# Kernel tuning notes

Measured on AMD Instinct MI355X. Metric: run time of the kernel, lower is better.

## Reference

```python
import jax, jax.numpy as jnp
import numpy as np

B_SZ, L, H, P, V, OUT_LEN = 32, 4096, 512, 384, 32, 16
DT_MIN, DT_MAX = 0.001, 0.1


def setup_inputs() -> dict:
    key = jax.random.key(0)
    ks = jax.random.split(key, 12)
    tokens = jax.random.randint(ks[0], (B_SZ, L), 0, V, dtype=jnp.int32)
    embed = jax.random.normal(ks[1], (V, H), dtype=jnp.float32) * 0.02
    # S5 diagonal state: Lambda = Lambda_re + i*Lambda_im (stable: Re < 0)
    Lambda_re = -0.5 * jax.random.uniform(ks[2], (P,), dtype=jnp.float32) - 1e-3
    Lambda_im = jnp.pi * jnp.arange(P, dtype=jnp.float32)
    B_re = jax.random.normal(ks[3], (P, H), dtype=jnp.float32) / np.sqrt(H)
    B_im = jax.random.normal(ks[4], (P, H), dtype=jnp.float32) / np.sqrt(H)
    C_re = jax.random.normal(ks[5], (H, P), dtype=jnp.float32) / np.sqrt(P)
    C_im = jax.random.normal(ks[6], (H, P), dtype=jnp.float32) / np.sqrt(P)
    D = jax.random.normal(ks[7], (H,), dtype=jnp.float32)
    log_step = jax.random.uniform(
        ks[8], (P,), dtype=jnp.float32,
        minval=np.log(DT_MIN), maxval=np.log(DT_MAX))
    W1 = jax.random.normal(ks[9], (H, H), dtype=jnp.float32) / np.sqrt(H)
    b1 = jnp.zeros((H,), dtype=jnp.float32)
    W2 = jax.random.normal(ks[10], (H, V), dtype=jnp.float32) / np.sqrt(H)
    b2 = jnp.zeros((V,), dtype=jnp.float32)
    return dict(tokens=tokens, embed=embed, Lambda_re=Lambda_re,
                Lambda_im=Lambda_im, B_re=B_re, B_im=B_im, C_re=C_re,
                C_im=C_im, D=D, log_step=log_step, W1=W1, b1=b1, W2=W2, b2=b2)


def _s5_scan(Lbar, Bu_bar):
    # Lbar: (P,) complex; Bu_bar: (B,L,P) complex
    A = jnp.broadcast_to(Lbar, Bu_bar.shape)

    def comb(e1, e2):
        A1, b1 = e1
        A2, b2 = e2
        return A2 * A1, A2 * b1 + b2

    _, xs = jax.lax.associative_scan(comb, (A, Bu_bar), axis=1)
    return xs  # (B,L,P) hidden states


def reference(tokens, embed, Lambda_re, Lambda_im, B_re, B_im,
              C_re, C_im, D, log_step, W1, b1, W2, b2):
    u = embed[tokens]                              # (B,L,H) real
    Lam = Lambda_re + 1j * Lambda_im               # (P,)
    step = jnp.exp(log_step)                       # (P,)
    Lbar = jnp.exp(Lam * step)                     # ZOH: exp(Lambda*dt)
    Bc = B_re + 1j * B_im                          # (P,H)
    Cc = C_re + 1j * C_im                          # (H,P)
    Bu = jnp.einsum('blh,ph->blp', u, Bc)          # (B,L,P) complex
    Bu_bar = ((Lbar - 1.0) / Lam) * Bu             # ZOH input discretization
    xs = _s5_scan(Lbar, Bu_bar)                    # (B,L,P)
    # conj_sym=True -> 2 * Re(C x) + D u
    y = 2.0 * jnp.einsum('blp,hp->blh', xs, Cc).real + u * D
    y = y[:, -OUT_LEN:, :]                         # (B,16,H)
    h = jax.nn.relu(y @ W1 + b1)
    return h @ W2 + b2                             # (B,16,V)
```

## Files before the change

### kernel.cpp

```cpp
#include <hip/hip_runtime.h>

#define B_SZ 32
#define L 4096
#define H 512
#define P 384
#define V 32
#define OUT_LEN 16
#define NC 48
#define CHUNK 85
#define T0 4080

#define OFF_DBL   0
#define OFF_LBARF 4608
#define OFF_WPOW  5376
#define OFF_M     79104
#define OFF_CT    103680
#define OFF_PART  496896
#define OFF_YT    1676544
#define OFF_HP    1938688

__global__ __launch_bounds__(256) void k_prep(
    const int* __restrict__ tokens, const float* __restrict__ embed,
    const float* __restrict__ Lre, const float* __restrict__ Lim,
    const float* __restrict__ Bre, const float* __restrict__ Bim,
    const float* __restrict__ Cre, const float* __restrict__ Cim,
    const float* __restrict__ log_step, float* __restrict__ ws)
{
    __shared__ float sre[32][33], sim[32][33];
    int bx = blockIdx.x, tid = threadIdx.x;
    if (bx < 2) {
        int p = bx * 256 + tid;
        if (p < P) {
            double dstep = exp((double)log_step[p]);
            double are = (double)Lre[p] * dstep, aim = (double)Lim[p] * dstep;
            double mag = exp(are);
            double lbr = mag * cos(aim), lbi = mag * sin(aim);
            double wmag = exp((double)CHUNK * are);
            double wang = (double)CHUNK * aim;
            double wr = wmag * cos(wang), wi = wmag * sin(wang);
            double lre = (double)Lre[p], lim = (double)Lim[p];
            double nr = lbr - 1.0, ni = lbi;
            double den = lre * lre + lim * lim;
            double cr = (nr * lre + ni * lim) / den, ci = (ni * lre - nr * lim) / den;
            double* d = (double*)ws + p * 6;
            d[0] = lbr; d[1] = lbi; d[2] = wr; d[3] = wi; d[4] = cr; d[5] = ci;
            ws[OFF_LBARF + 2 * p]     = (float)lbr;
            ws[OFF_LBARF + 2 * p + 1] = (float)lbi;
            double* wpow = (double*)(ws + OFF_WPOW);
            double awr = 1.0, awi = 0.0;
            for (int c = NC - 1; c >= 0; --c) {
                wpow[(c * P + p) * 2]     = awr;
                wpow[(c * P + p) * 2 + 1] = awi;
                double t = awr * wr - awi * wi;
                awi = awr * wi + awi * wr;
                awr = t;
            }
        }
    } else if (bx < 194) {
        int bxx = bx - 2;
        int tp = bxx >> 4, th = bxx & 15;
        int col = tid & 31, r0 = tid >> 5;
        #pragma unroll
        for (int it = 0; it < 4; ++it) {
            int row = r0 + 8 * it;
            int h = th * 32 + row, p = tp * 32 + col;
            sre[col][row] = Cre[h * P + p];
            sim[col][row] = Cim[h * P + p];
        }
        __syncthreads();
        #pragma unroll
        for (int it = 0; it < 4; ++it) {
            int pl = r0 + 8 * it;
            int p = tp * 32 + pl, h = th * 32 + col;
            ws[OFF_CT + (2 * p) * H + h]     = sre[pl][col];
            ws[OFF_CT + (2 * p + 1) * H + h] = sim[pl][col];
        }
    }
    {
        int w = bx * 4 + (tid >> 6);
        if (w < 1536) {
            int v0 = (w & 3) * 8, p = w >> 2;
            int lane = tid & 63;
            const float4* brp = (const float4*)(Bre + p * H);
            const float4* bip = (const float4*)(Bim + p * H);
            float4 br0 = brp[lane], br1 = brp[lane + 64];
            float4 bi0 = bip[lane], bi1 = bip[lane + 64];
            #pragma unroll
            for (int vv = 0; vv < 8; ++vv) {
                const float4* evp = (const float4*)(embed + (v0 + vv) * H);
                float4 e0 = evp[lane], e1 = evp[lane + 64];
                float dr = br0.x * e0.x;
                dr = fmaf(br0.y, e0.y, dr); dr = fmaf(br0.z, e0.z, dr);
                dr = fmaf(br0.w, e0.w, dr); dr = fmaf(br1.x, e1.x, dr);
                dr = fmaf(br1.y, e1.y, dr); dr = fmaf(br1.z, e1.z, dr);
                dr = fmaf(br1.w, e1.w, dr);
                float di = bi0.x * e0.x;
                di = fmaf(bi0.y, e0.y, di); di = fmaf(bi0.z, e0.z, di);
                di = fmaf(bi0.w, e0.w, di); di = fmaf(bi1.x, e1.x, di);
                di = fmaf(bi1.y, e1.y, di); di = fmaf(bi1.z, e1.z, di);
                di = fmaf(bi1.w, e1.w, di);
                #pragma unroll
                for (int off = 32; off; off >>= 1) {
                    dr += __shfl_down(dr, off);
                    di += __shfl_down(di, off);
                }
                if (lane == 0) {
                    ws[OFF_M + ((v0 + vv) * P + p) * 2]     = dr;
                    ws[OFF_M + ((v0 + vv) * P + p) * 2 + 1] = di;
                }
            }
        }
    }
}

__global__ __launch_bounds__(256) void k_scan(
    const int* __restrict__ tokens, const float* __restrict__ ws,
    float* __restrict__ part)
{
    __shared__ float2 sM[V * 192];
    int rem = blockIdx.x, b = blockIdx.y, tid = threadIdx.x;
    int ph = rem & 1;
    int c0 = (rem >> 1) * 4;
    const float2* Mg = (const float2*)(ws + OFF_M);
    for (int f = tid; f < V * 192; f += 256) {
        int v = f / 192, i = f - v * 192;
        sM[f] = Mg[v * P + ph * 192 + i];
    }
    __syncthreads();
    if (tid < 192) {
        int p = ph * 192 + tid;
        float Lr = ws[OFF_LBARF + 2 * p], Li = ws[OFF_LBARF + 2 * p + 1];
        const int* tk0 = tokens + b * L + (c0 + 0) * CHUNK;
        const int* tk1 = tokens + b * L + (c0 + 1) * CHUNK;
        const int* tk2 = tokens + b * L + (c0 + 2) * CHUNK;
        const int* tk3 = tokens + b * L + (c0 + 3) * CHUNK;
        float ar0 = 0, ai0 = 0, ar1 = 0, ai1 = 0;
        float ar2 = 0, ai2 = 0, ar3 = 0, ai3 = 0;
        for (int i = 0; i < CHUNK; ++i) {
            int t0 = tk0[i], t1 = tk1[i], t2 = tk2[i], t3 = tk3[i];
            float2 m0 = sM[t0 * 192 + tid];
            float2 m1 = sM[t1 * 192 + tid];
            float2 m2 = sM[t2 * 192 + tid];
            float2 m3 = sM[t3 * 192 + tid];
            float n;
            n = fmaf(Lr, ar0, fmaf(-Li, ai0, m0.x));
            ai0 = fmaf(Lr, ai0, fmaf(Li, ar0, m0.y)); ar0 = n;
            n = fmaf(Lr, ar1, fmaf(-Li, ai1, m1.x));
            ai1 = fmaf(Lr, ai1, fmaf(Li, ar1, m1.y)); ar1 = n;
            n = fmaf(Lr, ar2, fmaf(-Li, ai2, m2.x));
            ai2 = fmaf(Lr, ai2, fmaf(Li, ar2, m2.y)); ar2 = n;
            n = fmaf(Lr, ar3, fmaf(-Li, ai3, m3.x));
            ai3 = fmaf(Lr, ai3, fmaf(Li, ar3, m3.y)); ar3 = n;
        }
        const double* wpow = (const double*)(ws + OFF_WPOW);
        float* pt = part;
        #pragma unroll
        for (int k = 0; k < 4; ++k) {
            double wr = wpow[((c0 + k) * P + p) * 2];
            double wi = wpow[((c0 + k) * P + p) * 2 + 1];
            double ar = (k == 0) ? ar0 : (k == 1) ? ar1 : (k == 2) ? ar2 : ar3;
            double ai = (k == 0) ? ai0 : (k == 1) ? ai1 : (k == 2) ? ai2 : ai3;
            double sr = wr * ar - wi * ai;
            double si = wr * ai + wi * ar;
            pt[((b * NC + c0 + k) * P + p) * 2]     = (float)sr;
            pt[((b * NC + c0 + k) * P + p) * 2 + 1] = (float)si;
        }
    }
}

__global__ __launch_bounds__(256) void k_y(
    const int* __restrict__ tokens, const float* __restrict__ embed,
    const float* __restrict__ D, float* __restrict__ ws)
{
    __shared__ float sxs[P * 16];
    __shared__ float sred[4 * 64 * 9];
    int bx = blockIdx.x, tid = threadIdx.x;
    int b = bx >> 4, x = bx & 15;
    int lh = x & 1, hq = x >> 1;
    #pragma unroll
    for (int pass = 0; pass < 2; ++pass) {
        int p = tid + pass * 256;
        if (p < P) {
            const double* d = (const double*)ws + p * 6;
            double lbr = d[0], lbi = d[1], cr = d[4], ci = d[5];
            const float* pp = ws + OFF_PART + (b * NC * P + p) * 2;
            double s0r = 0, s0i = 0, s1r = 0, s1i = 0;
            double s2r = 0, s2i = 0, s3r = 0, s3i = 0;
            #pragma unroll
            for (int c = 0; c < NC; c += 4) {
                s0r += (double)pp[(c + 0) * P * 2];
                s0i += (double)pp[(c + 0) * P * 2 + 1];
                s1r += (double)pp[(c + 1) * P * 2];
                s1i += (double)pp[(c + 1) * P * 2 + 1];
                s2r += (double)pp[(c + 2) * P * 2];
                s2i += (double)pp[(c + 2) * P * 2 + 1];
                s3r += (double)pp[(c + 3) * P * 2];
                s3i += (double)pp[(c + 3) * P * 2 + 1];
            }
            double zr = (s0r + s1r) + (s2r + s3r);
            double zi = (s0i + s1i) + (s2i + s3i);
            const float* M0 = ws + OFF_M;
            const int* tk = tokens + b * L + T0;
            #pragma unroll
            for (int j = 0; j < OUT_LEN; ++j) {
                int t = tk[j];
                double mr = (double)M0[(t * P + p) * 2];
                double mi = (double)M0[(t * P + p) * 2 + 1];
                double tr = lbr * zr - lbi * zi + mr;
                double ti = lbr * zi + lbi * zr + mi;
                zr = tr; zi = ti;
                if ((j >> 3) == lh) {
                    int jl = j & 7;
                    sxs[p * 16 + 2 * jl]     = (float)(cr * zr - ci * zi);
                    sxs[p * 16 + 2 * jl + 1] = (float)(cr * zi + ci * zr);
                }
            }
        }
    }
    __syncthreads();
    int hl = tid & 63, pg = tid >> 6;
    int h = hq * 64 + hl;
    const float* ct = ws + OFF_CT;
    float acc[8];
    #pragma unroll
    for (int i = 0; i < 8; ++i) acc[i] = 0.f;
    int p0 = pg * 96;
    #pragma unroll 2
    for (int q = 0; q < 96; ++q) {
        int p = p0 + q;
        float cre = ct[(2 * p) * H + h];
        float cim = ct[(2 * p + 1) * H + h];
        const float4* xv = (const float4*)(sxs + p * 16);
        float4 x0 = xv[0], x1 = xv[1], x2 = xv[2], x3 = xv[3];
        acc[0] = fmaf(cre, x0.x, fmaf(-cim, x0.y, acc[0]));
        acc[1] = fmaf(cre, x0.z, fmaf(-cim, x0.w, acc[1]));
        acc[2] = fmaf(cre, x1.x, fmaf(-cim, x1.y, acc[2]));
        acc[3] = fmaf(cre, x1.z, fmaf(-cim, x1.w, acc[3]));
        acc[4] = fmaf(cre, x2.x, fmaf(-cim, x2.y, acc[4]));
        acc[5] = fmaf(cre, x2.z, fmaf(-cim, x2.w, acc[5]));
        acc[6] = fmaf(cre, x3.x, fmaf(-cim, x3.y, acc[6]));
        acc[7] = fmaf(cre, x3.z, fmaf(-cim, x3.w, acc[7]));
    }
    #pragma unroll
    for (int i = 0; i < 8; ++i)
        sred[(pg * 64 + hl) * 9 + i] = acc[i];
    __syncthreads();
    #pragma unroll
    for (int oo = 0; oo < 2; ++oo) {
        int o = tid + 256 * oo;
        int ohl = o & 63, oi = o >> 6;
        float s = sred[ohl * 9 + oi] + sred[(64 + ohl) * 9 + oi]
                + sred[(128 + ohl) * 9 + oi] + sred[(192 + ohl) * 9 + oi];
        int l = lh * 8 + oi;
        int t = tokens[b * L + T0 + l];
        int hh = hq * 64 + ohl;
        ws[OFF_YT + (b * OUT_LEN + l) * H + hh] =
            2.f * s + embed[t * H + hh] * D[hh];
    }
}

__global__ __launch_bounds__(256) void k_fc1(
    const float* __restrict__ W1, const float* __restrict__ ws,
    float* __restrict__ hp)
{
    __shared__ float ys[128 * 8];
    int bx = blockIdx.x, tid = threadIdx.x;
    int rg = bx >> 3, jh = (bx >> 2) & 1, kc = bx & 3;
    int j = jh * 256 + tid;
    int r0 = rg * 8, k0 = kc * 128;
    const float* yt = ws + OFF_YT;
    int kk = tid & 127, rr = tid >> 7;
    #pragma unroll
    for (int it = 0; it < 4; ++it)
        ys[kk * 8 + rr + 2 * it] = yt[(r0 + rr + 2 * it) * H + k0 + kk];
    __syncthreads();
    const float* wp = W1 + k0 * H + j;
    float wreg[8];
    #pragma unroll
    for (int u = 0; u < 8; ++u) wreg[u] = wp[u * H];
    float acc[8] = {0, 0, 0, 0, 0, 0, 0, 0};
    for (int kb = 0; kb < 128; kb += 8) {
        float cur[8];
        #pragma unroll
        for (int u = 0; u < 8; ++u) cur[u] = wreg[u];
        if (kb + 8 < 128) {
            #pragma unroll
            for (int u = 0; u < 8; ++u) wreg[u] = wp[(kb + 8 + u) * H];
        }
        #pragma unroll
        for (int u = 0; u < 8; ++u) {
            const float4* y0 = (const float4*)(ys + (kb + u) * 8);
            float4 p0 = y0[0], p1 = y0[1];
            float a = cur[u];
            acc[0] = fmaf(p0.x, a, acc[0]);
            acc[1] = fmaf(p0.y, a, acc[1]);
            acc[2] = fmaf(p0.z, a, acc[2]);
            acc[3] = fmaf(p0.w, a, acc[3]);
            acc[4] = fmaf(p1.x, a, acc[4]);
            acc[5] = fmaf(p1.y, a, acc[5]);
            acc[6] = fmaf(p1.z, a, acc[6]);
            acc[7] = fmaf(p1.w, a, acc[7]);
        }
    }
    #pragma unroll
    for (int i = 0; i < 8; ++i)
        hp[(kc * 512 + r0 + i) * H + j] = acc[i];
}

__global__ __launch_bounds__(256) void k_fc2(
    const float* __restrict__ b1, const float* __restrict__ W2,
    const float* __restrict__ b2, const float* __restrict__ hp,
    float* __restrict__ out)
{
    __shared__ float sh[512];
    __shared__ float red[8 * 32];
    int r = blockIdx.x, tid = threadIdx.x;
    #pragma unroll
    for (int half = 0; half < 2; ++half) {
        int j = half * 256 + tid;
        float s = b1[j] + hp[r * H + j] + hp[(512 + r) * H + j]
                        + hp[(1024 + r) * H + j] + hp[(1536 + r) * H + j];
        sh[j] = fmaxf(s, 0.f);
    }
    __syncthreads();
    int seg = tid >> 5, o = tid & 31;
    const float* w2 = W2 + seg * 64 * V + o;
    const float* hv = sh + seg * 64;
    float a0 = 0.f, a1 = 0.f, a2 = 0.f, a3 = 0.f;
    #pragma unroll
    for (int q = 0; q < 16; ++q) {
        a0 = fmaf(hv[q],      w2[q * V],        a0);
        a1 = fmaf(hv[16 + q], w2[(16 + q) * V], a1);
        a2 = fmaf(hv[32 + q], w2[(32 + q) * V], a2);
        a3 = fmaf(hv[48 + q], w2[(48 + q) * V], a3);
    }
    red[seg * 32 + o] = (a0 + a1) + (a2 + a3);
    __syncthreads();
    if (tid < 32) {
        float s = b2[tid];
        #pragma unroll
        for (int ss = 0; ss < 8; ++ss) s += red[ss * 32 + tid];
        out[r * V + tid] = s;
    }
}

extern "C" void kernel_launch(void* const* d_in, const int* in_sizes, int n_in,
                              void* d_out, int out_size, void* d_ws, size_t ws_size,
                              hipStream_t stream)
{
    const int*   tokens = (const int*)d_in[0];
    const float* embed  = (const float*)d_in[1];
    const float* Lre    = (const float*)d_in[2];
    const float* Lim    = (const float*)d_in[3];
    const float* Bre    = (const float*)d_in[4];
    const float* Bim    = (const float*)d_in[5];
    const float* Cre    = (const float*)d_in[6];
    const float* Cim    = (const float*)d_in[7];
    const float* D      = (const float*)d_in[8];
    const float* lstep  = (const float*)d_in[9];
    const float* W1     = (const float*)d_in[10];
    const float* b1     = (const float*)d_in[11];
    const float* W2     = (const float*)d_in[12];
    const float* b2     = (const float*)d_in[13];
    float* out = (float*)d_out;
    float* ws  = (float*)d_ws;

    k_prep<<<384, 256, 0, stream>>>(tokens, embed, Lre, Lim, Bre, Bim,
                                    Cre, Cim, lstep, ws);
    k_scan<<<dim3(24, 32), 256, 0, stream>>>(tokens, ws, ws + OFF_PART);
    k_y   <<<512, 256, 0, stream>>>(tokens, embed, D, ws);
    k_fc1 <<<512, 256, 0, stream>>>(W1, ws, ws + OFF_HP);
    k_fc2 <<<512, 256, 0, stream>>>(b1, W2, b2, ws + OFF_HP, out);
}
```

Baseline: 148.0 us.

## Interleave scan by stride-4 lanes, reduce superchunks via atomics, prefetch C in k_y

The scan now splits each sequence into 12 superchunks of 340 tokens. Each superchunk is processed as four interleaved sub-sequences, using Lbar^4 as the recurrence factor and reading tokens with int4 loads. The four partial states are recombined in double precision with powers of Lbar, weighted by the superchunk power, and summed with float atomicAdd into a per-batch accumulator. This replaces the per-chunk partial array and the 48-way reduction in k_y. The C-projection loop in k_y also gains software prefetching of C values. The risks are atomic contention, run-to-run nondeterminism in the sum, and the accuracy of float Lbar^4 over long runs.

```diff
diff --git a/kernel.cpp b/kernel.cpp
--- a/kernel.cpp
+++ b/kernel.cpp
@@ -6,21 +6,22 @@
 #define P 384
 #define V 32
 #define OUT_LEN 16
-#define NC 48
-#define CHUNK 85
+#define NSC 12
+#define SCLEN 340
+#define NSTEP 85
 #define T0 4080
 
 #define OFF_DBL   0
-#define OFF_LBARF 4608
+#define OFF_LBF4  4608
 #define OFF_WPOW  5376
-#define OFF_M     79104
-#define OFF_CT    103680
-#define OFF_PART  496896
-#define OFF_YT    1676544
-#define OFF_HP    1938688
+#define OFF_M     23808
+#define OFF_CT    48384
+#define OFF_XACC  441600
+#define OFF_YT    466176
+#define OFF_HP    728320
 
 __global__ __launch_bounds__(256) void k_prep(
-    const int* __restrict__ tokens, const float* __restrict__ embed,
+    const float* __restrict__ embed,
     const float* __restrict__ Lre, const float* __restrict__ Lim,
     const float* __restrict__ Bre, const float* __restrict__ Bim,
     const float* __restrict__ Cre, const float* __restrict__ Cim,
@@ -28,6 +29,7 @@
 {
     __shared__ float sre[32][33], sim[32][33];
     int bx = blockIdx.x, tid = threadIdx.x;
+    if (bx < 96) ws[OFF_XACC + bx * 256 + tid] = 0.f;
     if (bx < 2) {
         int p = bx * 256 + tid;
         if (p < P) {
@@ -35,20 +37,21 @@
             double are = (double)Lre[p] * dstep, aim = (double)Lim[p] * dstep;
             double mag = exp(are);
             double lbr = mag * cos(aim), lbi = mag * sin(aim);
-            double wmag = exp((double)CHUNK * are);
-            double wang = (double)CHUNK * aim;
-            double wr = wmag * cos(wang), wi = wmag * sin(wang);
             double lre = (double)Lre[p], lim = (double)Lim[p];
             double nr = lbr - 1.0, ni = lbi;
             double den = lre * lre + lim * lim;
             double cr = (nr * lre + ni * lim) / den, ci = (ni * lre - nr * lim) / den;
             double* d = (double*)ws + p * 6;
-            d[0] = lbr; d[1] = lbi; d[2] = wr; d[3] = wi; d[4] = cr; d[5] = ci;
-            ws[OFF_LBARF + 2 * p]     = (float)lbr;
-            ws[OFF_LBARF + 2 * p + 1] = (float)lbi;
+            d[0] = lbr; d[1] = lbi; d[2] = 0.0; d[3] = 0.0; d[4] = cr; d[5] = ci;
+            double m4 = exp(4.0 * are), a4 = 4.0 * aim;
+            ws[OFF_LBF4 + 2 * p]     = (float)(m4 * cos(a4));
+            ws[OFF_LBF4 + 2 * p + 1] = (float)(m4 * sin(a4));
+            double wmag = exp((double)SCLEN * are);
+            double wang = (double)SCLEN * aim;
+            double wr = wmag * cos(wang), wi = wmag * sin(wang);
             double* wpow = (double*)(ws + OFF_WPOW);
             double awr = 1.0, awi = 0.0;
-            for (int c = NC - 1; c >= 0; --c) {
+            for (int c = NSC - 1; c >= 0; --c) {
                 wpow[(c * P + p) * 2]     = awr;
                 wpow[(c * P + p) * 2 + 1] = awi;
                 double t = awr * wr - awi * wi;
@@ -114,13 +117,12 @@
 }
 
 __global__ __launch_bounds__(256) void k_scan(
-    const int* __restrict__ tokens, const float* __restrict__ ws,
-    float* __restrict__ part)
+    const int* __restrict__ tokens, float* __restrict__ ws)
 {
     __shared__ float2 sM[V * 192];
-    int rem = blockIdx.x, b = blockIdx.y, tid = threadIdx.x;
-    int ph = rem & 1;
-    int c0 = (rem >> 1) * 4;
+    int x = blockIdx.x, b = blockIdx.y, tid = threadIdx.x;
+    int ph = x & 1;
+    int sc = x >> 1;
     const float2* Mg = (const float2*)(ws + OFF_M);
     for (int f = tid; f < V * 192; f += 256) {
         int v = f / 192, i = f - v * 192;
@@ -129,19 +131,19 @@
     __syncthreads();
     if (tid < 192) {
         int p = ph * 192 + tid;
-        float Lr = ws[OFF_LBARF + 2 * p], Li = ws[OFF_LBARF + 2 * p + 1];
-        const int* tk0 = tokens + b * L + (c0 + 0) * CHUNK;
-        const int* tk1 = tokens + b * L + (c0 + 1) * CHUNK;
-        const int* tk2 = tokens + b * L + (c0 + 2) * CHUNK;
-        const int* tk3 = tokens + b * L + (c0 + 3) * CHUNK;
+        float Lr = ws[OFF_LBF4 + 2 * p], Li = ws[OFF_LBF4 + 2 * p + 1];
+        const int4* tkb = (const int4*)(tokens + b * L + sc * SCLEN);
         float ar0 = 0, ai0 = 0, ar1 = 0, ai1 = 0;
         float ar2 = 0, ai2 = 0, ar3 = 0, ai3 = 0;
-        for (int i = 0; i < CHUNK; ++i) {
-            int t0 = tk0[i], t1 = tk1[i], t2 = tk2[i], t3 = tk3[i];
-            float2 m0 = sM[t0 * 192 + tid];
-            float2 m1 = sM[t1 * 192 + tid];
-            float2 m2 = sM[t2 * 192 + tid];
-            float2 m3 = sM[t3 * 192 + tid];
+        int4 tq = tkb[0];
+        #pragma unroll 5
+        for (int i = 0; i < NSTEP; ++i) {
+            int4 cur = tq;
+            if (i + 1 < NSTEP) tq = tkb[i + 1];
+            float2 m0 = sM[cur.x * 192 + tid];
+            float2 m1 = sM[cur.y * 192 + tid];
+            float2 m2 = sM[cur.z * 192 + tid];
+            float2 m3 = sM[cur.w * 192 + tid];
             float n;
             n = fmaf(Lr, ar0, fmaf(-Li, ai0, m0.x));
             ai0 = fmaf(Lr, ai0, fmaf(Li, ar0, m0.y)); ar0 = n;
@@ -152,19 +154,20 @@
             n = fmaf(Lr, ar3, fmaf(-Li, ai3, m3.x));
             ai3 = fmaf(Lr, ai3, fmaf(Li, ar3, m3.y)); ar3 = n;
         }
+        const double* d = (const double*)ws + p * 6;
+        double l1r = d[0], l1i = d[1];
+        double l2r = l1r * l1r - l1i * l1i, l2i = 2.0 * l1r * l1i;
+        double l3r = l2r * l1r - l2i * l1i, l3i = l2r * l1i + l2i * l1r;
+        double zr = l3r * ar0 - l3i * ai0 + l2r * ar1 - l2i * ai1
+                  + l1r * ar2 - l1i * ai2 + (double)ar3;
+        double zi = l3r * ai0 + l3i * ar0 + l2r * ai1 + l2i * ar1
+                  + l1r * ai2 + l1i * ar2 + (double)ai3;
         const double* wpow = (const double*)(ws + OFF_WPOW);
-        float* pt = part;
-        #pragma unroll
-        for (int k = 0; k < 4; ++k) {
-            double wr = wpow[((c0 + k) * P + p) * 2];
-            double wi = wpow[((c0 + k) * P + p) * 2 + 1];
-            double ar = (k == 0) ? ar0 : (k == 1) ? ar1 : (k == 2) ? ar2 : ar3;
-            double ai = (k == 0) ? ai0 : (k == 1) ? ai1 : (k == 2) ? ai2 : ai3;
-            double sr = wr * ar - wi * ai;
-            double si = wr * ai + wi * ar;
-            pt[((b * NC + c0 + k) * P + p) * 2]     = (float)sr;
-            pt[((b * NC + c0 + k) * P + p) * 2 + 1] = (float)si;
-        }
+        double wr = wpow[(sc * P + p) * 2], wi = wpow[(sc * P + p) * 2 + 1];
+        float sr = (float)(wr * zr - wi * zi);
+        float si = (float)(wr * zi + wi * zr);
+        atomicAdd(ws + OFF_XACC + (b * P + p) * 2, sr);
+        atomicAdd(ws + OFF_XACC + (b * P + p) * 2 + 1, si);
     }
 }
 
@@ -183,22 +186,8 @@
         if (p < P) {
             const double* d = (const double*)ws + p * 6;
             double lbr = d[0], lbi = d[1], cr = d[4], ci = d[5];
-            const float* pp = ws + OFF_PART + (b * NC * P + p) * 2;
-            double s0r = 0, s0i = 0, s1r = 0, s1i = 0;
-            double s2r = 0, s2i = 0, s3r = 0, s3i = 0;
-            #pragma unroll
-            for (int c = 0; c < NC; c += 4) {
-                s0r += (double)pp[(c + 0) * P * 2];
-                s0i += (double)pp[(c + 0) * P * 2 + 1];
-                s1r += (double)pp[(c + 1) * P * 2];
-                s1i += (double)pp[(c + 1) * P * 2 + 1];
-                s2r += (double)pp[(c + 2) * P * 2];
-                s2i += (double)pp[(c + 2) * P * 2 + 1];
-                s3r += (double)pp[(c + 3) * P * 2];
-                s3i += (double)pp[(c + 3) * P * 2 + 1];
-            }
-            double zr = (s0r + s1r) + (s2r + s3r);
-            double zi = (s0i + s1i) + (s2i + s3i);
+            const float2 za = *(const float2*)(ws + OFF_XACC + (b * P + p) * 2);
+            double zr = (double)za.x, zi = (double)za.y;
             const float* M0 = ws + OFF_M;
             const int* tk = tokens + b * L + T0;
             #pragma unroll
@@ -225,21 +214,37 @@
     #pragma unroll
     for (int i = 0; i < 8; ++i) acc[i] = 0.f;
     int p0 = pg * 96;
-    #pragma unroll 2
-    for (int q = 0; q < 96; ++q) {
-        int p = p0 + q;
-        float cre = ct[(2 * p) * H + h];
-        float cim = ct[(2 * p + 1) * H + h];
-        const float4* xv = (const float4*)(sxs + p * 16);
-        float4 x0 = xv[0], x1 = xv[1], x2 = xv[2], x3 = xv[3];
-        acc[0] = fmaf(cre, x0.x, fmaf(-cim, x0.y, acc[0]));
-        acc[1] = fmaf(cre, x0.z, fmaf(-cim, x0.w, acc[1]));
-        acc[2] = fmaf(cre, x1.x, fmaf(-cim, x1.y, acc[2]));
-        acc[3] = fmaf(cre, x1.z, fmaf(-cim, x1.w, acc[3]));
-        acc[4] = fmaf(cre, x2.x, fmaf(-cim, x2.y, acc[4]));
-        acc[5] = fmaf(cre, x2.z, fmaf(-cim, x2.w, acc[5]));
-        acc[6] = fmaf(cre, x3.x, fmaf(-cim, x3.y, acc[6]));
-        acc[7] = fmaf(cre, x3.z, fmaf(-cim, x3.w, acc[7]));
+    float pr_[4], pi_[4];
+    #pragma unroll
+    for (int u = 0; u < 4; ++u) {
+        pr_[u] = ct[(2 * (p0 + u)) * H + h];
+        pi_[u] = ct[(2 * (p0 + u) + 1) * H + h];
+    }
+    for (int qs = 0; qs < 96; qs += 4) {
+        float cr_[4], ci_[4];
+        #pragma unroll
+        for (int u = 0; u < 4; ++u) { cr_[u] = pr_[u]; ci_[u] = pi_[u]; }
+        if (qs + 4 < 96) {
+            #pragma unroll
+            for (int u = 0; u < 4; ++u) {
+                pr_[u] = ct[(2 * (p0 + qs + 4 + u)) * H + h];
+                pi_[u] = ct[(2 * (p0 + qs + 4 + u) + 1) * H + h];
+            }
+        }
+        #pragma unroll
+        for (int u = 0; u < 4; ++u) {
+            const float4* xv = (const float4*)(sxs + (p0 + qs + u) * 16);
+            float4 x0 = xv[0], x1 = xv[1], x2 = xv[2], x3 = xv[3];
+            float cre = cr_[u], cim = ci_[u];
+            acc[0] = fmaf(cre, x0.x, fmaf(-cim, x0.y, acc[0]));
+            acc[1] = fmaf(cre, x0.z, fmaf(-cim, x0.w, acc[1]));
+            acc[2] = fmaf(cre, x1.x, fmaf(-cim, x1.y, acc[2]));
+            acc[3] = fmaf(cre, x1.z, fmaf(-cim, x1.w, acc[3]));
+            acc[4] = fmaf(cre, x2.x, fmaf(-cim, x2.y, acc[4]));
+            acc[5] = fmaf(cre, x2.z, fmaf(-cim, x2.w, acc[5]));
+            acc[6] = fmaf(cre, x3.x, fmaf(-cim, x3.y, acc[6]));
+            acc[7] = fmaf(cre, x3.z, fmaf(-cim, x3.w, acc[7]));
+        }
     }
     #pragma unroll
     for (int i = 0; i < 8; ++i)
@@ -365,9 +370,9 @@
     float* out = (float*)d_out;
     float* ws  = (float*)d_ws;
 
-    k_prep<<<384, 256, 0, stream>>>(tokens, embed, Lre, Lim, Bre, Bim,
+    k_prep<<<384, 256, 0, stream>>>(embed, Lre, Lim, Bre, Bim,
                                     Cre, Cim, lstep, ws);
-    k_scan<<<dim3(24, 32), 256, 0, stream>>>(tokens, ws, ws + OFF_PART);
+    k_scan<<<dim3(24, 32), 256, 0, stream>>>(tokens, ws);
     k_y   <<<512, 256, 0, stream>>>(tokens, embed, D, ws);
     k_fc1 <<<512, 256, 0, stream>>>(W1, ws, ws + OFF_HP);
     k_fc2 <<<512, 256, 0, stream>>>(b1, W2, b2, ws + OFF_HP, out);
```

After: 141.3 us (median of 2 runs). 4.6% less time.
